# Optimization experiments

Hardware: AMD Instinct MI355X
Metric: run time of the kernel (lower is better)

Reference implementation:

```python
import jax, jax.numpy as jnp
import numpy as np

B, S, HID, H, DH, WK, WV = 4, 1024, 1024, 16, 64, 64, 64

def setup_inputs() -> dict:
    key = jax.random.key(0)
    ks = jax.random.split(key, 10)
    sc = 0.02
    return {
        "hidden_states": jax.random.normal(ks[0], (B, S, HID), jnp.float32),
        "attention_mask": jnp.ones((B, S), jnp.float32),
        "Wq": jax.random.normal(ks[1], (H * DH, HID), jnp.float32) * sc,
        "bq": jnp.zeros((H * DH,), jnp.float32),
        "Wk": jax.random.normal(ks[2], (H * DH, HID), jnp.float32) * sc,
        "bk": jnp.zeros((H * DH,), jnp.float32),
        "Wv": jax.random.normal(ks[3], (H * DH, HID), jnp.float32) * sc,
        "bv": jnp.zeros((H * DH,), jnp.float32),
        "Wrk": jax.random.normal(ks[4], (2 * WK + 1, DH), jnp.float32) * sc,  # Linear(dh, 2wk+1) weight
        "Wrv": jax.random.normal(ks[5], (DH, 2 * WV + 1), jnp.float32) * sc,  # Linear(2wv+1, dh) weight
    }

def reference(hidden_states, attention_mask, Wq, bq, Wk, bk, Wv, bv, Wrk, Wrv):
    b, s, _ = hidden_states.shape
    dh = Wrk.shape[1]
    h = Wq.shape[0] // dh
    wk = (Wrk.shape[0] - 1) // 2
    wv = (Wrv.shape[1] - 1) // 2

    def proj(W, bias):
        return (hidden_states @ W.T + bias).reshape(b, s, h, dh).transpose(0, 2, 1, 3)

    q = proj(Wq, bq)  # [B,H,S,dh]
    k = proj(Wk, bk)
    v = proj(Wv, bv)

    # raw QK^T (no sqrt(d) scaling in this module)
    scores = jnp.einsum('bhnd,bhmd->bhnm', q, k)

    # relative-position key bias: scores_pos[i, i+d] = a_k[i, d+wk] for |d|<=wk
    a_k = jnp.einsum('bhnd,wd->bhnw', q, Wrk)  # [B,H,S,2wk+1]
    rel = jnp.arange(s)[None, :] - jnp.arange(s)[:, None] + wk  # [S,S]
    valid_k = (rel >= 0) & (rel < 2 * wk + 1)
    pos = jnp.take_along_axis(a_k, jnp.clip(rel, 0, 2 * wk)[None, None], axis=-1)
    scores = scores + jnp.where(valid_k[None, None], pos, 0.0)

    # attention mask: (1 - mask) * finfo.min added to scores
    min_val = jnp.finfo(scores.dtype).min
    scores = scores + (1.0 - attention_mask)[:, None, None, :] * min_val

    probs = jax.nn.softmax(scores, axis=-1)
    ctx = jnp.einsum('bhnm,bhmd->bhnd', probs, v)

    # relative-position value term: gather banded probs then Linear(2wv+1 -> dh)
    jcol = jnp.arange(s)[:, None] + jnp.arange(2 * wv + 1)[None, :] - wv  # [S,2wv+1]
    valid_v = (jcol >= 0) & (jcol < s)
    pp = jnp.take_along_axis(probs, jnp.clip(jcol, 0, s - 1)[None, None], axis=-1)
    pp = jnp.where(valid_v[None, None], pp, 0.0)  # [B,H,S,2wv+1]
    ctx = ctx + jnp.einsum('bhnw,dw->bhnd', pp, Wrv)

    return ctx.transpose(0, 2, 1, 3).reshape(b, s, h * dh)
```

## Files before the change

### kernel.cpp

```cpp
#include <hip/hip_runtime.h>
#include <stdint.h>

#define BB 4
#define SS 1024
#define HIDD 1024
#define NH 16
#define DHH 64

#define LOG2E 1.44269504f
#define MOFF  28.8539008f

typedef __attribute__((ext_vector_type(8))) short bf16x8;
typedef __attribute__((ext_vector_type(4))) float fx4;
typedef __attribute__((ext_vector_type(4))) int ix4;

__device__ __forceinline__ float bf2f(uint16_t u) {
    union { uint32_t u; float f; } x; x.u = ((uint32_t)u) << 16; return x.f;
}
__device__ __forceinline__ uint16_t f2bf(float f) {
    uint32_t u = __builtin_bit_cast(uint32_t, f);
    u = u + 0x7fffu + ((u >> 16) & 1u);
    return (uint16_t)(u >> 16);
}
__device__ __forceinline__ uint32_t pk_bf16(float lo, float hi) {
    uint32_t r;
    asm volatile("v_cvt_pk_bf16_f32 %0, %1, %2" : "=v"(r) : "v"(lo), "v"(hi));
    return r;
}
__device__ __forceinline__ float exp2_hw(float x) {
    float r;
    asm("v_exp_f32 %0, %1" : "=v"(r) : "v"(x));
    return r;
}
__device__ __forceinline__ bf16x8 mk_frag(uint32_t u0, uint32_t u1, uint32_t u2, uint32_t u3) {
    ix4 v = { (int)u0, (int)u1, (int)u2, (int)u3 };
    return __builtin_bit_cast(bf16x8, v);
}

__global__ __launch_bounds__(256) void cvt_kernel(const float* __restrict__ in,
                                                  uint16_t* __restrict__ out, int n) {
    int i = (blockIdx.x * 256 + threadIdx.x) * 4;
    if (i < n) {
        float4 v = *(const float4*)(in + i);
        uint2 p;
        p.x = pk_bf16(v.x, v.y);
        p.y = pk_bf16(v.z, v.w);
        *(uint2*)(out + i) = p;
    }
}

__global__ __launch_bounds__(256) void cvt3_kernel(const float* __restrict__ a,
                                                   const float* __restrict__ b,
                                                   const float* __restrict__ c,
                                                   uint16_t* __restrict__ oa,
                                                   uint16_t* __restrict__ ob,
                                                   uint16_t* __restrict__ oc) {
    const float* in = (blockIdx.y == 0) ? a : (blockIdx.y == 1) ? b : c;
    uint16_t* out = (blockIdx.y == 0) ? oa : (blockIdx.y == 1) ? ob : oc;
    int i = (blockIdx.x * 256 + threadIdx.x) * 4;
    float4 v = *(const float4*)(in + i);
    uint2 p;
    p.x = pk_bf16(v.x, v.y);
    p.y = pk_bf16(v.z, v.w);
    *(uint2*)(out + i) = p;
}

__global__ __launch_bounds__(256) void proj_gemm3(const uint16_t* __restrict__ X,
                                                  const uint16_t* __restrict__ Wq,
                                                  const uint16_t* __restrict__ Wk,
                                                  const uint16_t* __restrict__ Wv,
                                                  const float* __restrict__ bq,
                                                  const float* __restrict__ bk,
                                                  const float* __restrict__ bv,
                                                  uint16_t* __restrict__ oq,
                                                  uint16_t* __restrict__ ok,
                                                  uint16_t* __restrict__ ov) {
    const int z = blockIdx.z;
    const uint16_t* W = (z == 0) ? Wq : (z == 1) ? Wk : Wv;
    const float* bias = (z == 0) ? bq : (z == 1) ? bk : bv;
    uint16_t* out = (z == 0) ? oq : (z == 1) ? ok : ov;
    const float scl = (z == 0) ? LOG2E : 1.0f;

    __shared__ uint16_t Alds[128 * 64];
    __shared__ uint16_t Blds[128 * 64];
    const int tid = threadIdx.x;
    const int lane = tid & 63;
    const int wvi = tid >> 6;
    const int q16 = lane & 15;
    const int hh = lane >> 4;
    const int m0 = blockIdx.x * 128;
    const int n0 = blockIdx.y * 128;
    const int wr = wvi >> 1, wc = wvi & 1;

    fx4 zero4 = { 0.f, 0.f, 0.f, 0.f };
    fx4 acc[4][4];
    #pragma unroll
    for (int a = 0; a < 4; a++)
        #pragma unroll
        for (int c = 0; c < 4; c++) acc[a][c] = zero4;

    const int srow = tid >> 1, shalf = tid & 1;
    for (int k0 = 0; k0 < HIDD; k0 += 64) {
        const uint16_t* gA = X + (size_t)(m0 + srow) * HIDD + k0 + shalf * 32;
        const uint16_t* gB = W + (size_t)(n0 + srow) * HIDD + k0 + shalf * 32;
        #pragma unroll
        for (int i = 0; i < 4; i++) {
            uint4 va = *(const uint4*)(gA + i * 8);
            uint4 vb = *(const uint4*)(gB + i * 8);
            uint32_t bo = (uint32_t)((shalf * 64 + i * 16) ^ ((srow & 7) << 4));
            *(uint4*)((char*)Alds + srow * 128 + bo) = va;
            *(uint4*)((char*)Blds + srow * 128 + bo) = vb;
        }
        __syncthreads();
        #pragma unroll
        for (int kk = 0; kk < 2; kk++) {
            bf16x8 af[4], bfr[4];
            #pragma unroll
            for (int mi = 0; mi < 4; mi++) {
                int mr = wr * 64 + mi * 16 + q16;
                af[mi] = *(const bf16x8*)((char*)Alds + mr * 128 + ((kk * 64 + hh * 16) ^ ((mr & 7) << 4)));
            }
            #pragma unroll
            for (int ni = 0; ni < 4; ni++) {
                int nr = wc * 64 + ni * 16 + q16;
                bfr[ni] = *(const bf16x8*)((char*)Blds + nr * 128 + ((kk * 64 + hh * 16) ^ ((nr & 7) << 4)));
            }
            #pragma unroll
            for (int mi = 0; mi < 4; mi++)
                #pragma unroll
                for (int ni = 0; ni < 4; ni++)
                    acc[mi][ni] = __builtin_amdgcn_mfma_f32_16x16x32_bf16(af[mi], bfr[ni], acc[mi][ni], 0, 0, 0);
        }
        __syncthreads();
    }
    #pragma unroll
    for (int ni = 0; ni < 4; ni++) {
        int n = n0 + wc * 64 + ni * 16 + q16;
        float bvv = bias[n];
        int h = n >> 6, d = n & 63;
        #pragma unroll
        for (int mi = 0; mi < 4; mi++) {
            #pragma unroll
            for (int r = 0; r < 4; r++) {
                int m = m0 + wr * 64 + mi * 16 + 4 * hh + r;
                int b = m >> 10, s = m & 1023;
                out[(size_t)b * (NH * SS * DHH) + (size_t)h * (SS * DHH) + s * DHH + d] =
                    f2bf((acc[mi][ni][r] + bvv) * scl);
            }
        }
    }
}

__global__ __launch_bounds__(256) void vtrans(const uint16_t* __restrict__ v,
                                              uint16_t* __restrict__ vt) {
    __shared__ uint16_t t[64][72];
    const int tid = threadIdx.x;
    const int bh = blockIdx.y;
    const int s0 = blockIdx.x * 64;
    {
        int sl = tid >> 2, doff = (tid & 3) * 16;
        const uint16_t* src = v + (size_t)(bh * SS + s0 + sl) * 64 + doff;
        uint4 a = *(const uint4*)src;
        uint4 b2 = *(const uint4*)(src + 8);
        *(uint4*)&t[sl][doff] = a;
        *(uint4*)&t[sl][doff + 8] = b2;
    }
    __syncthreads();
    {
        int d = tid >> 2, soff = (tid & 3) * 16;
        uint32_t w[8];
        #pragma unroll
        for (int i = 0; i < 8; i++) {
            uint32_t lo = t[soff + 2 * i][d];
            uint32_t hi = t[soff + 2 * i + 1][d];
            w[i] = lo | (hi << 16);
        }
        uint16_t* dst = vt + (size_t)(bh * 64 + d) * SS + s0 + soff;
        uint4 o1 = { w[0], w[1], w[2], w[3] };
        uint4 o2 = { w[4], w[5], w[6], w[7] };
        *(uint4*)dst = o1;
        *(uint4*)(dst + 8) = o2;
    }
}

__global__ __launch_bounds__(256) void attn_kernel(
    const uint16_t* __restrict__ qg,
    const uint16_t* __restrict__ kg,
    const uint16_t* __restrict__ vtg,
    const float* __restrict__ amask,
    const uint16_t* __restrict__ Wrkb,
    const float* __restrict__ Wrv,
    float* __restrict__ out)
{
    __shared__ __align__(16) char smem[37888];
    uint16_t* Klds = (uint16_t*)smem;
    uint16_t* Vlds = (uint16_t*)(smem + 8192);
    uint16_t (*sband)[136] = (uint16_t (*)[136])(smem + 16384);
    float* maskf = (float*)(smem + 33792);

    const int tid = threadIdx.x;
    const int lane = tid & 63;
    const int wv = tid >> 6;
    const int q16 = lane & 15;
    const int hh = lane >> 4;
    const int id = blockIdx.y * 16 + blockIdx.x;
    const int xcd = id & 7, slot = id >> 3;
    const int bh = xcd + 8 * (slot >> 4);
    const int qt = slot & 15;
    const int b = bh >> 4;
    const int h = bh & 15;
    const int q0 = qt * 64;
    const int ql = wv * 16 + q16;
    const int qglob = q0 + ql;

    const uint16_t* qbh = qg + (size_t)bh * (SS * 64);
    const uint16_t* kbh = kg + (size_t)bh * (SS * 64);
    const uint16_t* vbh = vtg + (size_t)bh * (64 * SS);

    bf16x8 qf[2];
    #pragma unroll
    for (int ks = 0; ks < 2; ks++)
        qf[ks] = *(const bf16x8*)(qbh + (size_t)qglob * 64 + ks * 32 + hh * 8);

    const int srow = tid >> 2, spart = tid & 3;
    const uint32_t sb0 = (uint32_t)((spart * 32) ^ ((srow & 7) << 4));
    const uint32_t sb1 = (uint32_t)((spart * 32 + 16) ^ ((srow & 7) << 4));
    const uint16_t* gk0 = kbh + (size_t)srow * 64 + spart * 16;
    const uint16_t* gv0 = vbh + (size_t)srow * SS + spart * 16;
    uint4 ka  = *(const uint4*)gk0;
    uint4 kb2 = *(const uint4*)(gk0 + 8);
    uint4 va  = *(const uint4*)gv0;
    uint4 vb2 = *(const uint4*)(gv0 + 8);

    for (int i = tid * 4; i < SS; i += 1024) {
        float4 mv = *(const float4*)(amask + b * SS + i);
        fx4 o;
        o[0] = (1.0f - mv.x) * -2.0e38f - MOFF;
        o[1] = (1.0f - mv.y) * -2.0e38f - MOFF;
        o[2] = (1.0f - mv.z) * -2.0e38f - MOFF;
        o[3] = (1.0f - mv.w) * -2.0e38f - MOFF;
        *(fx4*)&maskf[i] = o;
    }

    #pragma unroll 1
    for (int wg = 0; wg < 9; wg++) {
        fx4 a = { 0.f, 0.f, 0.f, 0.f };
        int wrow = wg * 16 + q16; if (wrow > 128) wrow = 128;
        #pragma unroll
        for (int ks = 0; ks < 2; ks++) {
            bf16x8 af = *(const bf16x8*)(Wrkb + wrow * 64 + ks * 32 + hh * 8);
            a = __builtin_amdgcn_mfma_f32_16x16x32_bf16(af, qf[ks], a, 0, 0, 0);
        }
        if (wg < 8) {
            uint2 pp;
            pp.x = pk_bf16(a[0], a[1]);
            pp.y = pk_bf16(a[2], a[3]);
            *(uint2*)&sband[ql][wg * 16 + 4 * hh] = pp;
        } else if (hh == 0) {
            sband[ql][128] = f2bf(a[0]);
        }
    }
    if (qt == 0 || qt == 15) {
        int oend = hh * 33 + 33; if (oend > 129) oend = 129;
        for (int o = hh * 33; o < oend; o++) {
            int col = qglob + o - 64;
            if (col < 0 || col >= SS) sband[ql][o] = 0xff7f;
        }
    }
    __syncthreads();

    float lsum = 0.f;
    fx4 acc[4];
    #pragma unroll
    for (int dg = 0; dg < 4; dg++) acc[dg] = fx4{ 0.f, 0.f, 0.f, 0.f };

    const int srcA = q16 + 16 * ((2 * hh) & 3);
    const int srcB = q16 + 16 * ((2 * hh + 1) & 3);
    const bool lo = (hh < 2);

    for (int jt = 0; jt < 16; jt++) {
        *(uint4*)((char*)Klds + srow * 128 + sb0) = ka;
        *(uint4*)((char*)Klds + srow * 128 + sb1) = kb2;
        *(uint4*)((char*)Vlds + srow * 128 + sb0) = va;
        *(uint4*)((char*)Vlds + srow * 128 + sb1) = vb2;
        __syncthreads();

        if (jt < 15) {
            ka  = *(const uint4*)(gk0 + (size_t)(jt + 1) * 4096);
            kb2 = *(const uint4*)(gk0 + (size_t)(jt + 1) * 4096 + 8);
            va  = *(const uint4*)(gv0 + (jt + 1) * 64);
            vb2 = *(const uint4*)(gv0 + (jt + 1) * 64 + 8);
        }

        const int dj = jt - qt;
        const bool band = (dj >= -1) && (dj <= 1);
        uint32_t pk[4][2];
        #pragma unroll
        for (int mg = 0; mg < 4; mg++) {
            int mr = mg * 16 + q16;
            bf16x8 kf0 = *(const bf16x8*)((char*)Klds + mr * 128 + ((hh * 16) ^ ((mr & 7) << 4)));
            bf16x8 kf1 = *(const bf16x8*)((char*)Klds + mr * 128 + ((64 + hh * 16) ^ ((mr & 7) << 4)));
            fx4 s4 = { 0.f, 0.f, 0.f, 0.f };
            s4 = __builtin_amdgcn_mfma_f32_16x16x32_bf16(kf0, qf[0], s4, 0, 0, 0);
            s4 = __builtin_amdgcn_mfma_f32_16x16x32_bf16(kf1, qf[1], s4, 0, 0, 0);
            int mb = jt * 64 + mg * 16 + 4 * hh;
            fx4 mk4 = *(const fx4*)&maskf[mb];
            float p[4];
            #pragma unroll
            for (int r = 0; r < 4; r++) {
                int m = mb + r;
                float s = s4[r] + mk4[r];
                int o = m - qglob + 64;
                bool inb = band && (o >= 0) && (o <= 128);
                if (inb) {
                    s += bf2f(sband[ql][o]);
                    sband[ql][o] = f2bf(s + MOFF);
                }
                p[r] = exp2_hw(s);
            }
            lsum += (p[0] + p[1]) + (p[2] + p[3]);
            pk[mg][0] = pk_bf16(p[0], p[1]);
            pk[mg][1] = pk_bf16(p[2], p[3]);
        }

        #pragma unroll
        for (int ks = 0; ks < 2; ks++) {
            uint32_t a0 = (uint32_t)__shfl((int)pk[2 * ks][0], srcA);
            uint32_t b0 = (uint32_t)__shfl((int)pk[2 * ks + 1][0], srcA);
            uint32_t a1 = (uint32_t)__shfl((int)pk[2 * ks][1], srcA);
            uint32_t b1 = (uint32_t)__shfl((int)pk[2 * ks + 1][1], srcA);
            uint32_t a2 = (uint32_t)__shfl((int)pk[2 * ks][0], srcB);
            uint32_t b2 = (uint32_t)__shfl((int)pk[2 * ks + 1][0], srcB);
            uint32_t a3 = (uint32_t)__shfl((int)pk[2 * ks][1], srcB);
            uint32_t b3 = (uint32_t)__shfl((int)pk[2 * ks + 1][1], srcB);
            bf16x8 pf = mk_frag(lo ? a0 : b0, lo ? a1 : b1, lo ? a2 : b2, lo ? a3 : b3);
            #pragma unroll
            for (int dg = 0; dg < 4; dg++) {
                int dr = dg * 16 + q16;
                bf16x8 vf = *(const bf16x8*)((char*)Vlds + dr * 128 + ((ks * 64 + hh * 16) ^ ((dr & 7) << 4)));
                acc[dg] = __builtin_amdgcn_mfma_f32_16x16x32_bf16(vf, pf, acc[dg], 0, 0, 0);
            }
        }
        __syncthreads();
    }

    lsum += __shfl_xor(lsum, 16);
    lsum += __shfl_xor(lsum, 32);

    {
        int r = tid >> 2, c4 = tid & 3;
        const float* src = Wrv + r * 129 + c4 * 32;
        #pragma unroll
        for (int i = 0; i < 4; i++) {
            float4 f0 = *(const float4*)(src + i * 8);
            float4 f1 = *(const float4*)(src + i * 8 + 4);
            uint4 pkv;
            pkv.x = pk_bf16(f0.x, f0.y);
            pkv.y = pk_bf16(f0.z, f0.w);
            pkv.z = pk_bf16(f1.x, f1.y);
            pkv.w = pk_bf16(f1.z, f1.w);
            *(uint4*)(smem + r * 256 + ((c4 * 64 + i * 16) ^ ((r & 7) << 4))) = pkv;
        }
    }
    __syncthreads();

    #pragma unroll 1
    for (int ks = 0; ks < 4; ks++) {
        uint4 raw = *(const uint4*)((char*)sband + ql * 272 + ks * 64 + hh * 16);
        uint32_t rr[4] = { raw.x, raw.y, raw.z, raw.w };
        uint32_t eu[4];
        #pragma unroll
        for (int i = 0; i < 4; i++) {
            float e0 = exp2_hw(bf2f((uint16_t)(rr[i] & 0xffff)) - MOFF);
            float e1 = exp2_hw(bf2f((uint16_t)(rr[i] >> 16)) - MOFF);
            eu[i] = pk_bf16(e0, e1);
        }
        bf16x8 ef = mk_frag(eu[0], eu[1], eu[2], eu[3]);
        #pragma unroll
        for (int dg = 0; dg < 4; dg++) {
            int dr = dg * 16 + q16;
            bf16x8 wf = *(const bf16x8*)(smem + dr * 256 + ((ks * 64 + hh * 16) ^ ((dr & 7) << 4)));
            acc[dg] = __builtin_amdgcn_mfma_f32_16x16x32_bf16(wf, ef, acc[dg], 0, 0, 0);
        }
    }
    {
        float e128 = exp2_hw(bf2f(sband[ql][128]) - MOFF);
        #pragma unroll
        for (int dg = 0; dg < 4; dg++)
            #pragma unroll
            for (int r = 0; r < 4; r++)
                acc[dg][r] += e128 * Wrv[(dg * 16 + 4 * hh + r) * 129 + 128];
    }

    float inv_l = 1.0f / lsum;
    #pragma unroll
    for (int dg = 0; dg < 4; dg++) {
        fx4 o4 = acc[dg] * inv_l;
        int d0 = dg * 16 + 4 * hh;
        *(fx4*)(out + (size_t)(b * SS + qglob) * (NH * DHH) + h * DHH + d0) = o4;
    }
}

extern "C" void kernel_launch(void* const* d_in, const int* in_sizes, int n_in,
                              void* d_out, int out_size, void* d_ws, size_t ws_size,
                              hipStream_t stream) {
    const float* hs    = (const float*)d_in[0];
    const float* amask = (const float*)d_in[1];
    const float* Wq    = (const float*)d_in[2];
    const float* bq    = (const float*)d_in[3];
    const float* Wk    = (const float*)d_in[4];
    const float* bk    = (const float*)d_in[5];
    const float* Wv    = (const float*)d_in[6];
    const float* bv    = (const float*)d_in[7];
    const float* Wrk   = (const float*)d_in[8];
    const float* Wrv   = (const float*)d_in[9];
    float* out = (float*)d_out;

    char* ws = (char*)d_ws;
    uint16_t* Xb   = (uint16_t*)(ws + (0ull  << 20));
    uint16_t* Wqb  = (uint16_t*)(ws + (8ull  << 20));
    uint16_t* Wkb  = (uint16_t*)(ws + (10ull << 20));
    uint16_t* Wvb  = (uint16_t*)(ws + (12ull << 20));
    uint16_t* qw   = (uint16_t*)(ws + (14ull << 20));
    uint16_t* kw   = (uint16_t*)(ws + (22ull << 20));
    uint16_t* vw   = (uint16_t*)(ws + (30ull << 20));
    uint16_t* vtw  = (uint16_t*)(ws + (38ull << 20));
    uint16_t* Wrkb = (uint16_t*)(ws + (46ull << 20));

    cvt_kernel<<<4096, 256, 0, stream>>>(hs, Xb, 4096 * 1024);
    cvt3_kernel<<<dim3(1024, 3), 256, 0, stream>>>(Wq, Wk, Wv, Wqb, Wkb, Wvb);
    cvt_kernel<<<9, 256, 0, stream>>>(Wrk, Wrkb, 129 * 64);

    proj_gemm3<<<dim3(32, 8, 3), 256, 0, stream>>>(Xb, Wqb, Wkb, Wvb, bq, bk, bv, qw, kw, vw);

    vtrans<<<dim3(16, 64), 256, 0, stream>>>(vw, vtw);

    attn_kernel<<<dim3(16, 64), 256, 0, stream>>>(qw, kw, vtw, amask, Wrkb, Wrv, out);
}
```

Baseline: 123.1 us.

## Fuse conversions, prefetch GEMM tiles, write V transposed directly

Merges the three fp32-to-bf16 conversion launches into one kernel, which saves launch overhead. It adds register prefetch of the next K tile in the projection GEMM so global loads overlap the MFMA work. It also has the V projection write its output already transposed, which removes the separate vtrans kernel and a full round trip of V through memory. The trade-offs are higher register pressure in the GEMM and extra branching in the conversion kernel.

```diff
diff --git a/kernel.cpp b/kernel.cpp
--- a/kernel.cpp
+++ b/kernel.cpp
@@ -37,32 +37,29 @@
     return __builtin_bit_cast(bf16x8, v);
 }
 
-__global__ __launch_bounds__(256) void cvt_kernel(const float* __restrict__ in,
-                                                  uint16_t* __restrict__ out, int n) {
-    int i = (blockIdx.x * 256 + threadIdx.x) * 4;
-    if (i < n) {
-        float4 v = *(const float4*)(in + i);
-        uint2 p;
-        p.x = pk_bf16(v.x, v.y);
-        p.y = pk_bf16(v.z, v.w);
-        *(uint2*)(out + i) = p;
-    }
-}
-
-__global__ __launch_bounds__(256) void cvt3_kernel(const float* __restrict__ a,
-                                                   const float* __restrict__ b,
-                                                   const float* __restrict__ c,
-                                                   uint16_t* __restrict__ oa,
-                                                   uint16_t* __restrict__ ob,
-                                                   uint16_t* __restrict__ oc) {
-    const float* in = (blockIdx.y == 0) ? a : (blockIdx.y == 1) ? b : c;
-    uint16_t* out = (blockIdx.y == 0) ? oa : (blockIdx.y == 1) ? ob : oc;
-    int i = (blockIdx.x * 256 + threadIdx.x) * 4;
-    float4 v = *(const float4*)(in + i);
+__global__ __launch_bounds__(256) void cvt_all(const float* __restrict__ x,
+                                               const float* __restrict__ wq,
+                                               const float* __restrict__ wk,
+                                               const float* __restrict__ wv,
+                                               const float* __restrict__ wrk,
+                                               uint16_t* __restrict__ xb,
+                                               uint16_t* __restrict__ wqb,
+                                               uint16_t* __restrict__ wkb,
+                                               uint16_t* __restrict__ wvb,
+                                               uint16_t* __restrict__ wrkb) {
+    long i = ((long)blockIdx.x * 256 + threadIdx.x) * 4;
+    const float* in; uint16_t* out; long off;
+    if (i < 4194304)      { in = x;   out = xb;   off = i; }
+    else if (i < 5242880) { in = wq;  out = wqb;  off = i - 4194304; }
+    else if (i < 6291456) { in = wk;  out = wkb;  off = i - 5242880; }
+    else if (i < 7340032) { in = wv;  out = wvb;  off = i - 6291456; }
+    else if (i < 7348288) { in = wrk; out = wrkb; off = i - 7340032; }
+    else return;
+    float4 v = *(const float4*)(in + off);
     uint2 p;
     p.x = pk_bf16(v.x, v.y);
     p.y = pk_bf16(v.z, v.w);
-    *(uint2*)(out + i) = p;
+    *(uint2*)(out + off) = p;
 }
 
 __global__ __launch_bounds__(256) void proj_gemm3(const uint16_t* __restrict__ X,
@@ -100,18 +97,30 @@
         for (int c = 0; c < 4; c++) acc[a][c] = zero4;
 
     const int srow = tid >> 1, shalf = tid & 1;
+    const uint16_t* gA = X + (size_t)(m0 + srow) * HIDD + shalf * 32;
+    const uint16_t* gB = W + (size_t)(n0 + srow) * HIDD + shalf * 32;
+    uint4 ar[4], br[4];
+    #pragma unroll
+    for (int i = 0; i < 4; i++) {
+        ar[i] = *(const uint4*)(gA + i * 8);
+        br[i] = *(const uint4*)(gB + i * 8);
+    }
+
     for (int k0 = 0; k0 < HIDD; k0 += 64) {
-        const uint16_t* gA = X + (size_t)(m0 + srow) * HIDD + k0 + shalf * 32;
-        const uint16_t* gB = W + (size_t)(n0 + srow) * HIDD + k0 + shalf * 32;
         #pragma unroll
         for (int i = 0; i < 4; i++) {
-            uint4 va = *(const uint4*)(gA + i * 8);
-            uint4 vb = *(const uint4*)(gB + i * 8);
             uint32_t bo = (uint32_t)((shalf * 64 + i * 16) ^ ((srow & 7) << 4));
-            *(uint4*)((char*)Alds + srow * 128 + bo) = va;
-            *(uint4*)((char*)Blds + srow * 128 + bo) = vb;
+            *(uint4*)((char*)Alds + srow * 128 + bo) = ar[i];
+            *(uint4*)((char*)Blds + srow * 128 + bo) = br[i];
         }
         __syncthreads();
+        if (k0 < HIDD - 64) {
+            #pragma unroll
+            for (int i = 0; i < 4; i++) {
+                ar[i] = *(const uint4*)(gA + k0 + 64 + i * 8);
+                br[i] = *(const uint4*)(gB + k0 + 64 + i * 8);
+            }
+        }
         #pragma unroll
         for (int kk = 0; kk < 2; kk++) {
             bf16x8 af[4], bfr[4];
@@ -133,53 +142,41 @@
         }
         __syncthreads();
     }
-    #pragma unroll
-    for (int ni = 0; ni < 4; ni++) {
-        int n = n0 + wc * 64 + ni * 16 + q16;
-        float bvv = bias[n];
-        int h = n >> 6, d = n & 63;
-        #pragma unroll
-        for (int mi = 0; mi < 4; mi++) {
-            #pragma unroll
-            for (int r = 0; r < 4; r++) {
-                int m = m0 + wr * 64 + mi * 16 + 4 * hh + r;
-                int b = m >> 10, s = m & 1023;
-                out[(size_t)b * (NH * SS * DHH) + (size_t)h * (SS * DHH) + s * DHH + d] =
-                    f2bf((acc[mi][ni][r] + bvv) * scl);
-            }
-        }
-    }
-}
-
-__global__ __launch_bounds__(256) void vtrans(const uint16_t* __restrict__ v,
-                                              uint16_t* __restrict__ vt) {
-    __shared__ uint16_t t[64][72];
-    const int tid = threadIdx.x;
-    const int bh = blockIdx.y;
-    const int s0 = blockIdx.x * 64;
-    {
-        int sl = tid >> 2, doff = (tid & 3) * 16;
-        const uint16_t* src = v + (size_t)(bh * SS + s0 + sl) * 64 + doff;
-        uint4 a = *(const uint4*)src;
-        uint4 b2 = *(const uint4*)(src + 8);
-        *(uint4*)&t[sl][doff] = a;
-        *(uint4*)&t[sl][doff + 8] = b2;
-    }
-    __syncthreads();
-    {
-        int d = tid >> 2, soff = (tid & 3) * 16;
-        uint32_t w[8];
-        #pragma unroll
-        for (int i = 0; i < 8; i++) {
-            uint32_t lo = t[soff + 2 * i][d];
-            uint32_t hi = t[soff + 2 * i + 1][d];
-            w[i] = lo | (hi << 16);
-        }
-        uint16_t* dst = vt + (size_t)(bh * 64 + d) * SS + s0 + soff;
-        uint4 o1 = { w[0], w[1], w[2], w[3] };
-        uint4 o2 = { w[4], w[5], w[6], w[7] };
-        *(uint4*)dst = o1;
-        *(uint4*)(dst + 8) = o2;
+
+    if (z < 2) {
+        #pragma unroll
+        for (int ni = 0; ni < 4; ni++) {
+            int n = n0 + wc * 64 + ni * 16 + q16;
+            float bvv = bias[n];
+            int h = n >> 6, d = n & 63;
+            #pragma unroll
+            for (int mi = 0; mi < 4; mi++) {
+                #pragma unroll
+                for (int r = 0; r < 4; r++) {
+                    int m = m0 + wr * 64 + mi * 16 + 4 * hh + r;
+                    int b = m >> 10, s = m & 1023;
+                    out[(size_t)b * (NH * SS * DHH) + (size_t)h * (SS * DHH) + s * DHH + d] =
+                        f2bf((acc[mi][ni][r] + bvv) * scl);
+                }
+            }
+        }
+    } else {
+        int b = m0 >> 10;
+        int sbase = (m0 & 1023) + wr * 64;
+        #pragma unroll
+        for (int ni = 0; ni < 4; ni++) {
+            int n = n0 + wc * 64 + ni * 16 + q16;
+            float bvv = bias[n];
+            int h = n >> 6, d = n & 63;
+            uint16_t* base = out + ((size_t)(b * 16 + h) * 64 + d) * SS + sbase;
+            #pragma unroll
+            for (int mi = 0; mi < 4; mi++) {
+                uint2 pp;
+                pp.x = pk_bf16(acc[mi][ni][0] + bvv, acc[mi][ni][1] + bvv);
+                pp.y = pk_bf16(acc[mi][ni][2] + bvv, acc[mi][ni][3] + bvv);
+                *(uint2*)(base + mi * 16 + 4 * hh) = pp;
+            }
+        }
     }
 }
 
@@ -423,17 +420,12 @@
     uint16_t* Wvb  = (uint16_t*)(ws + (12ull << 20));
     uint16_t* qw   = (uint16_t*)(ws + (14ull << 20));
     uint16_t* kw   = (uint16_t*)(ws + (22ull << 20));
-    uint16_t* vw   = (uint16_t*)(ws + (30ull << 20));
     uint16_t* vtw  = (uint16_t*)(ws + (38ull << 20));
     uint16_t* Wrkb = (uint16_t*)(ws + (46ull << 20));
 
-    cvt_kernel<<<4096, 256, 0, stream>>>(hs, Xb, 4096 * 1024);
-    cvt3_kernel<<<dim3(1024, 3), 256, 0, stream>>>(Wq, Wk, Wv, Wqb, Wkb, Wvb);
-    cvt_kernel<<<9, 256, 0, stream>>>(Wrk, Wrkb, 129 * 64);
-
-    proj_gemm3<<<dim3(32, 8, 3), 256, 0, stream>>>(Xb, Wqb, Wkb, Wvb, bq, bk, bv, qw, kw, vw);
-
-    vtrans<<<dim3(16, 64), 256, 0, stream>>>(vw, vtw);
+    cvt_all<<<7177, 256, 0, stream>>>(hs, Wq, Wk, Wv, Wrk, Xb, Wqb, Wkb, Wvb, Wrkb);
+
+    proj_gemm3<<<dim3(32, 8, 3), 256, 0, stream>>>(Xb, Wqb, Wkb, Wvb, bq, bk, bv, qw, kw, vtw);
 
     attn_kernel<<<dim3(16, 64), 256, 0, stream>>>(qw, kw, vtw, amask, Wrkb, Wrv, out);
 }
```

After: 184.8 us. 1.5x slower.
